# Performance work log

Hardware: AMD Instinct MI355X
Metric: run time of the kernel (lower is better)

Reference implementation:

```python
import jax, jax.numpy as jnp
import numpy as np

B, S, DIM, NH, NKV, HD, HID, L, VOCAB = 1, 2048, 1024, 16, 8, 64, 2816, 2, 32000
EPS = 1e-5
SCALE = float(HD) ** 0.5
NEG = -255.0  # mask fill value used by executorch example inputs


def setup_inputs() -> dict:
    key = jax.random.key(0)
    ks = jax.random.split(key, 16)
    sd = 0.02
    def rnd(k, shape):
        return jax.random.normal(k, shape, dtype=jnp.float32) * sd
    # rope tables: precompute_freqs_cis(head_dim, max_seq_len)[: -1] -> [S, HD//2]
    inv = 1.0 / (10000.0 ** (np.arange(0, HD, 2, dtype=np.float32) / HD))
    ang = np.outer(np.arange(S, dtype=np.float32), inv)
    # causal mask [S, S]
    tril = np.tril(np.ones((S, S), dtype=bool))
    mask = np.where(tril, 0.0, NEG).astype(np.float32)
    return {
        "tokens": jax.random.randint(ks[0], (B, S), 0, VOCAB, dtype=jnp.int32),
        "atten_mask": jnp.asarray(mask),
        "freqs_cos": jnp.asarray(np.cos(ang)),
        "freqs_sin": jnp.asarray(np.sin(ang)),
        "tok_emb": rnd(ks[1], (VOCAB, DIM)),
        "wq": rnd(ks[2], (L, DIM, NH * HD)),
        "wk": rnd(ks[3], (L, DIM, NKV * HD)),
        "wv": rnd(ks[4], (L, DIM, NKV * HD)),
        "wo": rnd(ks[5], (L, NH * HD, DIM)),
        "attn_norm_w": jnp.ones((L, DIM), jnp.float32),
        "ffn_norm_w": jnp.ones((L, DIM), jnp.float32),
        "w1": rnd(ks[6], (L, DIM, HID)),
        "w2": rnd(ks[7], (L, HID, DIM)),
        "w3": rnd(ks[8], (L, DIM, HID)),
        "final_norm_w": jnp.ones((DIM,), jnp.float32),
        "out_w": rnd(ks[9], (DIM, VOCAB)),
    }


def _rmsnorm(x, w):
    return x * jax.lax.rsqrt(jnp.mean(x * x, axis=-1, keepdims=True) + EPS) * w


def _rope(x, c, s):
    # faithful to apply_rotary_emb_single: de-interleave, rotate, concat halves
    xr, xi = x[..., ::2], x[..., 1::2]          # [B,S,H,HD/2]
    c = c[None, :, None, :]
    s = s[None, :, None, :]
    return jnp.concatenate([xr * c - xi * s, xr * s + xi * c], axis=-1)


def reference(tokens, atten_mask, freqs_cos, freqs_sin, tok_emb, wq, wk, wv, wo,
              attn_norm_w, ffn_norm_w, w1, w2, w3, final_norm_w, out_w):
    rep = NH // NKV
    h = tok_emb[tokens]                           # [B,S,DIM]
    k_news, v_news = [], []
    for l in range(L):
        x = _rmsnorm(h, attn_norm_w[l])
        q = (x @ wq[l]).reshape(B, S, NH, HD)
        k = (x @ wk[l]).reshape(B, S, NKV, HD)
        v = (x @ wv[l]).reshape(B, S, NKV, HD)
        q = _rope(q, freqs_cos, freqs_sin)
        k = _rope(k, freqs_cos, freqs_sin)
        # GQA: each kv head serves NH//NKV query heads
        kr = jnp.repeat(k, rep, axis=2)           # [B,S,NH,HD]
        vr = jnp.repeat(v, rep, axis=2)
        attn = jnp.einsum('bshd,bthd->bhst', q, kr) / SCALE + atten_mask[None, None]
        p = jax.nn.softmax(attn, axis=-1)
        y = jnp.einsum('bhst,bthd->bshd', p, vr).reshape(B, S, NH * HD)
        h = h + y @ wo[l]
        x = _rmsnorm(h, ffn_norm_w[l])
        h = h + (jax.nn.silu(x @ w1[l]) * (x @ w3[l])) @ w2[l]
        # output_new_cache_only: last-position rotated K and raw V per kv head
        k_news.append(k[:, -1])                   # [B,NKV,HD]
        v_news.append(v[:, -1])
    logits = _rmsnorm(h, final_norm_w) @ out_w    # [B,S,VOCAB]
    return logits, jnp.stack(k_news), jnp.stack(v_news)
```

## Files before the change

kernel.cpp:

```cpp
#include <hip/hip_runtime.h>
#include <hip/hip_bf16.h>

typedef __bf16 bf16x8 __attribute__((ext_vector_type(8)));
typedef float f32x4 __attribute__((ext_vector_type(4)));
typedef unsigned short ushort4v __attribute__((ext_vector_type(4)));
typedef unsigned short ushort8v __attribute__((ext_vector_type(8)));

#define S_LEN 2048
#define DIM 1024
#define NH 16
#define NKV 8
#define HD 64
#define HID 2816

__device__ __forceinline__ unsigned short f2bf(float f) {
    union { float f; unsigned u; } v; v.f = f;
    unsigned r = v.u + 0x7fffu + ((v.u >> 16) & 1u);
    return (unsigned short)(r >> 16);
}
__device__ __forceinline__ float bf2f(unsigned short u) {
    union { unsigned u; float f; } v; v.u = (unsigned)u << 16; return v.f;
}

__device__ __forceinline__ void gload16(const unsigned short* g, unsigned short* l) {
    __builtin_amdgcn_global_load_lds(
        (const __attribute__((address_space(1))) unsigned int*)g,
        (__attribute__((address_space(3))) unsigned int*)l,
        16, 0, 0);
}

union Frag { f32x4 f; bf16x8 h; };

__device__ __forceinline__ f32x4 lds_read_b128(unsigned addr) {
    f32x4 d;
    asm volatile("ds_read_b128 %0, %1" : "=v"(d) : "v"(addr));
    return d;
}

#define BAR()  asm volatile("s_barrier" ::: "memory")
#define WAITV(n) asm volatile("s_waitcnt vmcnt(" #n ")" ::: "memory")
#define LGKM0() do { asm volatile("s_waitcnt lgkmcnt(0)" ::: "memory"); __builtin_amdgcn_sched_barrier(0); } while (0)

__global__ __launch_bounds__(256) void embed_kernel(const int* __restrict__ tokens,
                                                    const float* __restrict__ emb,
                                                    float* __restrict__ h) {
    int s = blockIdx.x;
    int t = tokens[s];
    float4 v = *(const float4*)&emb[(size_t)t * DIM + threadIdx.x * 4];
    *(float4*)&h[(size_t)s * DIM + threadIdx.x * 4] = v;
}

__global__ __launch_bounds__(256) void rmsnorm_kernel(const float* __restrict__ x,
                                                      const float* __restrict__ w,
                                                      unsigned short* __restrict__ out) {
    __shared__ float sred[4];
    int s = blockIdx.x;
    int tid = threadIdx.x;
    float4 v = *(const float4*)&x[(size_t)s * DIM + tid * 4];
    float ss = v.x * v.x + v.y * v.y + v.z * v.z + v.w * v.w;
#pragma unroll
    for (int off = 32; off; off >>= 1) ss += __shfl_down(ss, off);
    if ((tid & 63) == 0) sred[tid >> 6] = ss;
    __syncthreads();
    float tot = sred[0] + sred[1] + sred[2] + sred[3];
    float scale = rsqrtf(tot * (1.0f / DIM) + 1e-5f);
    float4 wv = *(const float4*)&w[tid * 4];
    ushort4v o;
    o[0] = f2bf(v.x * scale * wv.x); o[1] = f2bf(v.y * scale * wv.y);
    o[2] = f2bf(v.z * scale * wv.z); o[3] = f2bf(v.w * scale * wv.w);
    *(ushort4v*)&out[(size_t)s * DIM + tid * 4] = o;
}

__global__ __launch_bounds__(256) void transpose_w(const float* __restrict__ in,
                                                   unsigned short* __restrict__ out,
                                                   int K, int N) {
    __shared__ unsigned short t[64][68];
    int n0 = blockIdx.x * 64, k0 = blockIdx.y * 64;
    int tid = threadIdx.x;
    int tn = tid & 15, tk = tid >> 4;
#pragma unroll
    for (int p = 0; p < 4; ++p) {
        int k = tk + p * 16;
        float4 v = *(const float4*)&in[(size_t)(k0 + k) * N + n0 + tn * 4];
        t[tn * 4 + 0][k] = f2bf(v.x);
        t[tn * 4 + 1][k] = f2bf(v.y);
        t[tn * 4 + 2][k] = f2bf(v.z);
        t[tn * 4 + 3][k] = f2bf(v.w);
    }
    __syncthreads();
    int wk = tid & 15, wn = tid >> 4;
#pragma unroll
    for (int p = 0; p < 4; ++p) {
        int n = wn + p * 16;
        ushort4v v;
        v[0] = t[n][wk * 4]; v[1] = t[n][wk * 4 + 1];
        v[2] = t[n][wk * 4 + 2]; v[3] = t[n][wk * 4 + 3];
        *(ushort4v*)&out[(size_t)(n0 + n) * K + k0 + wk * 4] = v;
    }
}

__global__ __launch_bounds__(256) void transpose_v(const unsigned short* __restrict__ in,
                                                   unsigned short* __restrict__ out) {
    __shared__ unsigned short t[64][72];
    int c0 = blockIdx.x * 64, s0 = blockIdx.y * 64;
    int tid = threadIdx.x;
    int tc = tid & 15, ts = tid >> 4;
#pragma unroll
    for (int p = 0; p < 4; ++p) {
        int s = ts + p * 16;
        ushort4v v = *(const ushort4v*)&in[(size_t)(s0 + s) * 512 + c0 + tc * 4];
        t[tc * 4 + 0][s] = v[0];
        t[tc * 4 + 1][s] = v[1];
        t[tc * 4 + 2][s] = v[2];
        t[tc * 4 + 3][s] = v[3];
    }
    __syncthreads();
    int ws_ = tid & 15, wc = tid >> 4;
#pragma unroll
    for (int p = 0; p < 4; ++p) {
        int c = wc + p * 16;
        ushort4v v;
        v[0] = t[c][ws_ * 4]; v[1] = t[c][ws_ * 4 + 1];
        v[2] = t[c][ws_ * 4 + 2]; v[3] = t[c][ws_ * 4 + 3];
        *(ushort4v*)&out[(size_t)(c0 + c) * 2048 + s0 + ws_ * 4] = v;
    }
}

__global__ __launch_bounds__(256) void gemm_tn(const unsigned short* __restrict__ A, int lda,
                                               const unsigned short* __restrict__ Bt,
                                               float* __restrict__ Cf,
                                               unsigned short* __restrict__ Cb,
                                               const float* __restrict__ addsrc,
                                               int N, int K) {
    __shared__ unsigned short As[128 * 64];
    __shared__ unsigned short Bs[128 * 64];
    int tid = threadIdx.x;
    int lane = tid & 63;
    int wid = tid >> 6;
    int wrow = wid >> 1, wcol = wid & 1;
    int lr = lane & 15, lg = lane >> 4;
    const int m0 = blockIdx.x * 128, n0 = blockIdx.y * 128;

    const int col8 = (((lane & 7) ^ ((lane >> 3) & 7)) * 8);
    const unsigned short* aG = A + (size_t)(m0 + wid * 32 + (lane >> 3)) * lda + col8;
    const unsigned short* bG = Bt + (size_t)(n0 + wid * 32 + (lane >> 3)) * K + col8;
    unsigned short* aL = As + wid * 2048;
    unsigned short* bL = Bs + wid * 2048;

    f32x4 acc[4][4] = {};

    for (int k0 = 0; k0 < K; k0 += 64) {
#pragma unroll
        for (int i = 0; i < 4; ++i)
            gload16(aG + (size_t)(i * 8) * lda + k0, aL + i * 512);
#pragma unroll
        for (int i = 0; i < 4; ++i)
            gload16(bG + (size_t)(i * 8) * K + k0, bL + i * 512);
        __syncthreads();
#pragma unroll
        for (int kk = 0; kk < 2; ++kk) {
            const int slot = ((kk * 4 + lg) ^ (lr & 7)) * 8;
            bf16x8 aF[4], bF[4];
#pragma unroll
            for (int mi = 0; mi < 4; ++mi)
                aF[mi] = *(const bf16x8*)&As[(wrow * 64 + mi * 16 + lr) * 64 + slot];
#pragma unroll
            for (int ni = 0; ni < 4; ++ni)
                bF[ni] = *(const bf16x8*)&Bs[(wcol * 64 + ni * 16 + lr) * 64 + slot];
#pragma unroll
            for (int mi = 0; mi < 4; ++mi)
#pragma unroll
                for (int ni = 0; ni < 4; ++ni)
                    acc[mi][ni] = __builtin_amdgcn_mfma_f32_16x16x32_bf16(aF[mi], bF[ni], acc[mi][ni], 0, 0, 0);
        }
        __syncthreads();
    }
#pragma unroll
    for (int mi = 0; mi < 4; ++mi)
#pragma unroll
        for (int ni = 0; ni < 4; ++ni) {
            int row = m0 + wrow * 64 + mi * 16 + lg * 4;
            int col = n0 + wcol * 64 + ni * 16 + lr;
#pragma unroll
            for (int r = 0; r < 4; ++r) {
                size_t idx = (size_t)(row + r) * N + col;
                float v = acc[mi][ni][r];
                if (addsrc) v += addsrc[idx];
                if (Cb) Cb[idx] = f2bf(v);
                else    Cf[idx] = v;
            }
        }
}

__global__ __launch_bounds__(256) void gemm_tn64(const unsigned short* __restrict__ A, int lda,
                                                 const unsigned short* __restrict__ Bt,
                                                 float* __restrict__ Cf,
                                                 unsigned short* __restrict__ Cb,
                                                 const float* __restrict__ addsrc,
                                                 int N, int K) {
    __shared__ unsigned short As[64 * 64];
    __shared__ unsigned short Bs[128 * 64];
    int tid = threadIdx.x;
    int lane = tid & 63;
    int wid = tid >> 6;
    int lr = lane & 15, lg = lane >> 4;
    const int m0 = blockIdx.x * 64, n0 = blockIdx.y * 128;

    const int srow = tid >> 3;
    const int col8 = (((tid & 7) ^ ((tid >> 3) & 7)) * 8);
    const unsigned short* aG = A + (size_t)(m0 + srow) * lda + col8;
    const unsigned short* bG = Bt + (size_t)(n0 + srow) * K + col8;
    unsigned short* aL = As + wid * 512;
    unsigned short* bL = Bs + wid * 512;

    f32x4 acc[4][2] = {};

    for (int k0 = 0; k0 < K; k0 += 64) {
        gload16(aG + k0, aL);
        gload16(aG + (size_t)32 * lda + k0, aL + 2048);
#pragma unroll
        for (int i = 0; i < 4; ++i)
            gload16(bG + (size_t)(i * 32) * K + k0, bL + i * 2048);
        __syncthreads();
#pragma unroll
        for (int kk = 0; kk < 2; ++kk) {
            const int slot = ((kk * 4 + lg) ^ (lr & 7)) * 8;
            bf16x8 aF[4], bF[2];
#pragma unroll
            for (int mi = 0; mi < 4; ++mi)
                aF[mi] = *(const bf16x8*)&As[(mi * 16 + lr) * 64 + slot];
#pragma unroll
            for (int ni = 0; ni < 2; ++ni)
                bF[ni] = *(const bf16x8*)&Bs[(wid * 32 + ni * 16 + lr) * 64 + slot];
#pragma unroll
            for (int mi = 0; mi < 4; ++mi)
#pragma unroll
                for (int ni = 0; ni < 2; ++ni)
                    acc[mi][ni] = __builtin_amdgcn_mfma_f32_16x16x32_bf16(aF[mi], bF[ni], acc[mi][ni], 0, 0, 0);
        }
        __syncthreads();
    }
#pragma unroll
    for (int mi = 0; mi < 4; ++mi)
#pragma unroll
        for (int ni = 0; ni < 2; ++ni) {
            int row = m0 + mi * 16 + lg * 4;
            int col = n0 + wid * 32 + ni * 16 + lr;
#pragma unroll
            for (int r = 0; r < 4; ++r) {
                size_t idx = (size_t)(row + r) * N + col;
                float v = acc[mi][ni][r];
                if (addsrc) v += addsrc[idx];
                if (Cb) Cb[idx] = f2bf(v);
                else    Cf[idx] = v;
            }
        }
}

__global__ __launch_bounds__(512) void gemm8(const unsigned short* __restrict__ A,
                                             const unsigned short* __restrict__ Bt,
                                             float* __restrict__ Cf,
                                             unsigned short* __restrict__ Cb,
                                             int N, int K) {
    __shared__ unsigned short ldsbuf[65536];
    const int NT = K >> 6;
    int tid = threadIdx.x;
    int lane = tid & 63;
    int wid = tid >> 6;
    int wm = wid >> 2, wn = wid & 3;
    int lr = lane & 15, lg = lane >> 4;
    int wl = blockIdx.x * gridDim.y + blockIdx.y;
    const int m0 = (wl & 7) * 256, n0 = (wl >> 3) * 256;

    unsigned lds0 = (unsigned)(size_t)(__attribute__((address_space(3))) unsigned short*)ldsbuf;
    const unsigned xoff = (unsigned)((lg ^ ((lr >> 1) & 3)) * 16);
    const int gsw = (lane & 3) ^ ((lane >> 3) & 3);
    const int srow = wid * 16 + (lane >> 2);

#define STAGE(buf, ab, s, t) do {                                                   \
        const unsigned short* _src = (ab) ? Bt : A;                                 \
        int _r0 = (ab) ? n0 : m0;                                                   \
        unsigned short* _l = ldsbuf + (((buf) * 2 + (ab)) * 2 + (s)) * 8192 + wid * 512; \
        const unsigned short* _g = _src + (size_t)(_r0 + srow) * K + (size_t)(t) * 64 + (s) * 32 + gsw * 8; \
        gload16(_g, _l);                                                            \
        gload16(_g + (size_t)128 * K, _l + 4096);                                   \
    } while (0)

    f32x4 acc[8][4] = {};

    STAGE(0, 0, 0, 0); STAGE(0, 1, 0, 0);
    STAGE(0, 0, 1, 0); STAGE(0, 1, 1, 0);
    STAGE(1, 0, 0, 1); STAGE(1, 1, 0, 1);
    WAITV(8);
    BAR();

    for (int t = 0; t < NT; ++t) {
        int buf = t & 1;
        unsigned aBase = lds0 + (unsigned)(buf * 65536) + (unsigned)((wm * 128 + lr) * 64) + xoff;
        unsigned bBase = lds0 + (unsigned)(buf * 65536 + 32768) + (unsigned)((wn * 64 + lr) * 64) + xoff;
        Frag aF[4], bF[4];
#pragma unroll
        for (int s = 0; s < 2; ++s) {
#pragma unroll
            for (int ni = 0; ni < 4; ++ni)
                bF[ni].f = lds_read_b128(bBase + (unsigned)(s * 16384 + ni * 1024));
#pragma unroll
            for (int mi = 0; mi < 4; ++mi)
                aF[mi].f = lds_read_b128(aBase + (unsigned)(s * 16384 + mi * 1024));
            if (s == 0) { if (t + 1 < NT) STAGE(buf ^ 1, 0, 1, t + 1); }
            else        { if (t + 2 < NT) STAGE(buf,     0, 0, t + 2); }
            BAR();
            LGKM0();
            __builtin_amdgcn_s_setprio(1);
#pragma unroll
            for (int mi = 0; mi < 4; ++mi)
#pragma unroll
                for (int ni = 0; ni < 4; ++ni)
                    acc[mi][ni] = __builtin_amdgcn_mfma_f32_16x16x32_bf16(aF[mi].h, bF[ni].h, acc[mi][ni], 0, 0, 0);
            __builtin_amdgcn_s_setprio(0);
            BAR();
#pragma unroll
            for (int mi = 0; mi < 4; ++mi)
                aF[mi].f = lds_read_b128(aBase + (unsigned)(4096 + s * 16384 + mi * 1024));
            if (s == 0) { if (t + 1 < NT) STAGE(buf ^ 1, 1, 1, t + 1); }
            else        { if (t + 2 < NT) STAGE(buf,     1, 0, t + 2); }
            BAR();
            LGKM0();
            __builtin_amdgcn_s_setprio(1);
#pragma unroll
            for (int mi = 0; mi < 4; ++mi)
#pragma unroll
                for (int ni = 0; ni < 4; ++ni)
                    acc[4 + mi][ni] = __builtin_amdgcn_mfma_f32_16x16x32_bf16(aF[mi].h, bF[ni].h, acc[4 + mi][ni], 0, 0, 0);
            __builtin_amdgcn_s_setprio(0);
            if (s == 0) {
                if (t + 1 < NT) { WAITV(8); } else { WAITV(0); }
            } else {
                if (t + 2 < NT)      { WAITV(8); }
                else if (t + 1 < NT) { WAITV(4); }
            }
            BAR();
        }
    }
#undef STAGE

#pragma unroll
    for (int mi = 0; mi < 8; ++mi)
#pragma unroll
        for (int ni = 0; ni < 4; ++ni) {
            int row = m0 + wm * 128 + mi * 16 + lg * 4;
            int col = n0 + wn * 64 + ni * 16 + lr;
#pragma unroll
            for (int r = 0; r < 4; ++r) {
                size_t idx = (size_t)(row + r) * N + col;
                float v = acc[mi][ni][r];
                if (Cb) Cb[idx] = f2bf(v);
                else    Cf[idx] = v;
            }
        }
}

__global__ __launch_bounds__(256) void rope_kernel(const float* __restrict__ qkv,
                                                   const float* __restrict__ fc,
                                                   const float* __restrict__ fs,
                                                   unsigned short* __restrict__ qb,
                                                   unsigned short* __restrict__ kb,
                                                   unsigned short* __restrict__ vb,
                                                   float* __restrict__ out, int layer) {
    const size_t LOGITS = (size_t)S_LEN * 32000;
    int s = blockIdx.x * 4 + (threadIdx.x >> 6);
    int hh = blockIdx.y;
    int lane = threadIdx.x & 63;
    const float* base = qkv + (size_t)s * 2048;
    if (hh < NH) {
        if (lane < 32) {
            const float* row = base + hh * HD;
            float2 x2 = *(const float2*)&row[2 * lane];
            float c = fc[s * 32 + lane], sn = fs[s * 32 + lane];
            size_t o = (size_t)s * (NH * HD) + hh * HD + lane;
            qb[o] = f2bf(x2.x * c - x2.y * sn);
            qb[o + 32] = f2bf(x2.x * sn + x2.y * c);
        }
    } else if (hh < NH + NKV) {
        int kh = hh - NH;
        if (lane < 32) {
            const float* row = base + 1024 + kh * HD;
            float2 x2 = *(const float2*)&row[2 * lane];
            float c = fc[s * 32 + lane], sn = fs[s * 32 + lane];
            float o0 = x2.x * c - x2.y * sn, o1 = x2.x * sn + x2.y * c;
            size_t o = (size_t)s * (NKV * HD) + kh * HD + lane;
            kb[o] = f2bf(o0);
            kb[o + 32] = f2bf(o1);
            if (s == S_LEN - 1) {
                float* kn = out + LOGITS + (size_t)layer * (NKV * HD) + kh * HD;
                kn[lane] = o0; kn[lane + 32] = o1;
            }
        }
    } else {
        int vh = hh - NH - NKV;
        const float* row = base + 1536 + vh * HD;
        float val = row[lane];
        vb[(size_t)s * (NKV * HD) + vh * HD + lane] = f2bf(val);
        if (s == S_LEN - 1)
            out[LOGITS + (size_t)2 * (NKV * HD) + (size_t)layer * (NKV * HD) + vh * HD + lane] = val;
    }
}

__global__ __launch_bounds__(512) void attn_kernel(const unsigned short* __restrict__ qb,
                                                   const unsigned short* __restrict__ kb,
                                                   const unsigned short* __restrict__ vT,
                                                   unsigned short* __restrict__ yb) {
    __shared__ unsigned short Klds[2][4096];
    __shared__ unsigned short Vlds[2][4096];
    __shared__ unsigned short P[8][16 * 72];
    int kvh = blockIdx.x;
    int qt64 = blockIdx.y;
    int tid = threadIdx.x;
    int lane = tid & 63;
    int w = tid >> 6;
    int hq = w & 1, qsub = w >> 1;
    int h = kvh * 2 + hq;
    int lr = lane & 15, lg = lane >> 4;
    int qbase = qt64 * 64 + qsub * 16;
    int qrow = qbase + lr;

    const int sr = tid >> 3;
    const int scol8 = (((tid & 7) ^ ((tid >> 3) & 7)) * 8);
    const int NT = qt64 + 1;

#define STAGEKV(buf, kt) do { \
        gload16(&kb[(size_t)((kt) * 64 + sr) * (NKV * HD) + kvh * 64 + scol8], &Klds[buf][w * 512]); \
        gload16(&vT[(size_t)(kvh * 64 + sr) * 2048 + (kt) * 64 + scol8], &Vlds[buf][w * 512]); \
    } while (0)

    bf16x8 bq[2];
#pragma unroll
    for (int c = 0; c < 2; ++c)
        bq[c] = *(const bf16x8*)&qb[(size_t)qrow * (NH * HD) + h * HD + c * 32 + lg * 8];

    f32x4 O[4] = {};
    float mstate = -1e30f, lstate = 0.f;

    STAGEKV(0, 0);
    WAITV(0);
    BAR();

    for (int kt = 0; kt < NT; ++kt) {
        int buf = kt & 1;
        if (kt + 1 < NT) STAGEKV(buf ^ 1, kt + 1);
        f32x4 s[4];
#pragma unroll
        for (int kc = 0; kc < 4; ++kc) {
            int krl = kc * 16 + lr;
            const unsigned short* kp = &Klds[buf][krl * 64];
            bf16x8 ak0 = *(const bf16x8*)&kp[((lg ^ (lr & 7)) * 8)];
            bf16x8 ak1 = *(const bf16x8*)&kp[(((4 + lg) ^ (lr & 7)) * 8)];
            f32x4 z = {};
            z = __builtin_amdgcn_mfma_f32_16x16x32_bf16(ak0, bq[0], z, 0, 0, 0);
            z = __builtin_amdgcn_mfma_f32_16x16x32_bf16(ak1, bq[1], z, 0, 0, 0);
            s[kc] = z;
        }
        float tm = -1e30f;
#pragma unroll
        for (int kc = 0; kc < 4; ++kc)
#pragma unroll
            for (int r = 0; r < 4; ++r) {
                int key = kt * 64 + kc * 16 + lg * 4 + r;
                float val = s[kc][r] * 0.125f;
                if (key > qrow) val = -1e30f;
                s[kc][r] = val;
                tm = fmaxf(tm, val);
            }
        tm = fmaxf(tm, __shfl_xor(tm, 16));
        tm = fmaxf(tm, __shfl_xor(tm, 32));
        float mn = fmaxf(mstate, tm);
        float sc = __expf(mstate - mn);
        float rs = 0.f;
        ushort4v pk[4];
#pragma unroll
        for (int kc = 0; kc < 4; ++kc)
#pragma unroll
            for (int r = 0; r < 4; ++r) {
                float pf = __expf(s[kc][r] - mn);
                rs += pf;
                pk[kc][r] = f2bf(pf);
            }
        rs += __shfl_xor(rs, 16);
        rs += __shfl_xor(rs, 32);
        lstate = lstate * sc + rs;
        mstate = mn;
        float osc[4];
#pragma unroll
        for (int r = 0; r < 4; ++r)
            osc[r] = __shfl(sc, lg * 4 + r);
#pragma unroll
        for (int n = 0; n < 4; ++n)
#pragma unroll
            for (int r = 0; r < 4; ++r)
                O[n][r] *= osc[r];
#pragma unroll
        for (int kc = 0; kc < 4; ++kc)
            *(ushort4v*)&P[w][lr * 72 + kc * 16 + lg * 4] = pk[kc];
        bf16x8 pa[2];
#pragma unroll
        for (int g = 0; g < 2; ++g)
            pa[g] = *(const bf16x8*)&P[w][lr * 72 + g * 32 + lg * 8];
#pragma unroll
        for (int n = 0; n < 4; ++n) {
            const unsigned short* vp = &Vlds[buf][(n * 16 + lr) * 64];
#pragma unroll
            for (int g = 0; g < 2; ++g) {
                bf16x8 bv = *(const bf16x8*)&vp[(((g * 4 + lg) ^ (lr & 7)) * 8)];
                O[n] = __builtin_amdgcn_mfma_f32_16x16x32_bf16(pa[g], bv, O[n], 0, 0, 0);
            }
        }
        if (kt + 1 < NT) WAITV(0);
        LGKM0();
        BAR();
    }
#undef STAGEKV

    float linv[4];
#pragma unroll
    for (int r = 0; r < 4; ++r)
        linv[r] = 1.f / __shfl(lstate, lg * 4 + r);
#pragma unroll
    for (int n = 0; n < 4; ++n)
#pragma unroll
        for (int r = 0; r < 4; ++r) {
            int row = qbase + lg * 4 + r;
            yb[(size_t)row * (NH * HD) + h * HD + n * 16 + lr] = f2bf(O[n][r] * linv[r]);
        }
}

__global__ __launch_bounds__(256) void silu_mul_kernel(unsigned short* __restrict__ gu) {
    size_t idx = (size_t)blockIdx.x * 256 + threadIdx.x;
    int s = (int)(idx / 352);
    int c8 = (int)(idx % 352);
    unsigned short* gp = gu + (size_t)s * 5632 + c8 * 8;
    ushort8v a = *(const ushort8v*)gp;
    ushort8v b = *(const ushort8v*)(gp + 2816);
#pragma unroll
    for (int j = 0; j < 8; ++j) {
        float x = bf2f(a[j]), y = bf2f(b[j]);
        a[j] = f2bf(x / (1.f + __expf(-x)) * y);
    }
    *(ushort8v*)gp = a;
}

extern "C" void kernel_launch(void* const* d_in, const int* in_sizes, int n_in,
                              void* d_out, int out_size, void* d_ws, size_t ws_size,
                              hipStream_t stream) {
    const int* tokens = (const int*)d_in[0];
    const float* freqs_cos = (const float*)d_in[2];
    const float* freqs_sin = (const float*)d_in[3];
    const float* tok_emb = (const float*)d_in[4];
    const float* wq = (const float*)d_in[5];
    const float* wk = (const float*)d_in[6];
    const float* wv = (const float*)d_in[7];
    const float* wo = (const float*)d_in[8];
    const float* attn_norm_w = (const float*)d_in[9];
    const float* ffn_norm_w = (const float*)d_in[10];
    const float* w1 = (const float*)d_in[11];
    const float* w2 = (const float*)d_in[12];
    const float* w3 = (const float*)d_in[13];
    const float* final_norm_w = (const float*)d_in[14];
    const float* out_w = (const float*)d_in[15];
    float* out = (float*)d_out;

    const size_t SD = (size_t)S_LEN * DIM;
    const size_t SKV = (size_t)S_LEN * NKV * HD;

    char* p = (char*)d_ws;
    auto take = [&](size_t bytes) { char* r = p; p += (bytes + 255) & ~(size_t)255; return r; };
    float* h            = (float*)take(SD * 4);
    unsigned short* xnb = (unsigned short*)take(SD * 2);
    char* uni = p;
    float* qkvf         = (float*)uni;
    unsigned short* qb  = (unsigned short*)(uni + 17039360);
    unsigned short* kb  = qb + SD;
    unsigned short* vb  = kb + SKV;
    unsigned short* vT  = vb + SKV;
    unsigned short* ybv = vT + SKV;
    unsigned short* gu  = ybv + SD;
    unsigned short* wT  = gu + (size_t)S_LEN * 5632;
    unsigned short* owT = (unsigned short*)uni;

    embed_kernel<<<S_LEN, 256, 0, stream>>>(tokens, tok_emb, h);
    for (int l = 0; l < 2; ++l) {
        rmsnorm_kernel<<<S_LEN, 256, 0, stream>>>(h, attn_norm_w + l * DIM, xnb);
        transpose_w<<<dim3(16, 16), 256, 0, stream>>>(wq + (size_t)l * DIM * 1024, wT, DIM, 1024);
        transpose_w<<<dim3(8, 16), 256, 0, stream>>>(wk + (size_t)l * DIM * 512, wT + (size_t)1024 * DIM, DIM, 512);
        transpose_w<<<dim3(8, 16), 256, 0, stream>>>(wv + (size_t)l * DIM * 512, wT + (size_t)1536 * DIM, DIM, 512);
        gemm_tn<<<dim3(16, 16), 256, 0, stream>>>(xnb, DIM, wT, qkvf, nullptr, nullptr, 2048, DIM);
        rope_kernel<<<dim3(S_LEN / 4, 32), 256, 0, stream>>>(qkvf, freqs_cos, freqs_sin, qb, kb, vb, out, l);
        transpose_v<<<dim3(8, 32), 256, 0, stream>>>(vb, vT);
        attn_kernel<<<dim3(NKV, S_LEN / 64), 512, 0, stream>>>(qb, kb, vT, ybv);
        transpose_w<<<dim3(16, 16), 256, 0, stream>>>(wo + (size_t)l * 1024 * DIM, wT, 1024, DIM);
        gemm_tn64<<<dim3(32, 8), 256, 0, stream>>>(ybv, 1024, wT, h, nullptr, h, DIM, 1024);
        rmsnorm_kernel<<<S_LEN, 256, 0, stream>>>(h, ffn_norm_w + l * DIM, xnb);
        transpose_w<<<dim3(44, 16), 256, 0, stream>>>(w1 + (size_t)l * DIM * HID, wT, DIM, HID);
        transpose_w<<<dim3(44, 16), 256, 0, stream>>>(w3 + (size_t)l * DIM * HID, wT + (size_t)HID * DIM, DIM, HID);
        gemm8<<<dim3(8, 22), 512, 0, stream>>>(xnb, wT, nullptr, gu, 5632, DIM);
        silu_mul_kernel<<<(S_LEN * 352) / 256, 256, 0, stream>>>(gu);
        transpose_w<<<dim3(16, 44), 256, 0, stream>>>(w2 + (size_t)l * HID * 1024, wT, HID, 1024);
        gemm_tn64<<<dim3(32, 8), 256, 0, stream>>>(gu, 5632, wT, h, nullptr, h, DIM, HID);
    }
    rmsnorm_kernel<<<S_LEN, 256, 0, stream>>>(h, final_norm_w, xnb);
    transpose_w<<<dim3(500, 16), 256, 0, stream>>>(out_w, owT, DIM, 32000);
    gemm8<<<dim3(8, 125), 512, 0, stream>>>(xnb, owT, out, nullptr, 32000, DIM);
}
```

Baseline: 688.5 us.

## Fuse SiLU into FFN GEMM epilogue, merge transposes, retile attention

Several changes at once. The w1/w3 weights are interleaved row-wise so the gate/up GEMM epilogue can pair outputs with a lane shuffle and write silu(g)*u directly, which removes the separate silu kernel and halves the gu buffer. The q/k/v and w1/w3 weight transposes are merged into single launches, and the V conversion plus transpose now reads straight from the fp32 QKV output, which drops the vb round trip. Attention moves to 256-thread blocks over 32-row query strips, scheduled heaviest-first to balance causal work. The risk is lower per-block parallelism in attention and some wasted early-exit blocks in the merged qkv transpose.

```diff
diff --git a/kernel.cpp b/kernel.cpp
--- a/kernel.cpp
+++ b/kernel.cpp
@@ -12,6 +12,7 @@
 #define NKV 8
 #define HD 64
 #define HID 2816
+#define LOGITS ((size_t)S_LEN * 32000)
 
 __device__ __forceinline__ unsigned short f2bf(float f) {
     union { float f; unsigned u; } v; v.f = f;
@@ -71,11 +72,11 @@
     *(ushort4v*)&out[(size_t)s * DIM + tid * 4] = o;
 }
 
-__global__ __launch_bounds__(256) void transpose_w(const float* __restrict__ in,
-                                                   unsigned short* __restrict__ out,
-                                                   int K, int N) {
+__device__ __forceinline__ void tpose_body(const float* __restrict__ in,
+                                           unsigned short* __restrict__ out,
+                                           int K, int N, int n0, int k0,
+                                           int rowMul, int rowOff) {
     __shared__ unsigned short t[64][68];
-    int n0 = blockIdx.x * 64, k0 = blockIdx.y * 64;
     int tid = threadIdx.x;
     int tn = tid & 15, tk = tid >> 4;
 #pragma unroll
@@ -95,12 +96,38 @@
         ushort4v v;
         v[0] = t[n][wk * 4]; v[1] = t[n][wk * 4 + 1];
         v[2] = t[n][wk * 4 + 2]; v[3] = t[n][wk * 4 + 3];
-        *(ushort4v*)&out[(size_t)(n0 + n) * K + k0 + wk * 4] = v;
-    }
-}
-
-__global__ __launch_bounds__(256) void transpose_v(const unsigned short* __restrict__ in,
-                                                   unsigned short* __restrict__ out) {
+        *(ushort4v*)&out[(size_t)(rowMul * (n0 + n) + rowOff) * K + k0 + wk * 4] = v;
+    }
+}
+
+__global__ __launch_bounds__(256) void transpose_w(const float* __restrict__ in,
+                                                   unsigned short* __restrict__ out,
+                                                   int K, int N) {
+    tpose_body(in, out, K, N, blockIdx.x * 64, blockIdx.y * 64, 1, 0);
+}
+
+__global__ __launch_bounds__(256) void transpose_qkv(const float* __restrict__ wq,
+                                                     const float* __restrict__ wk,
+                                                     const float* __restrict__ wv,
+                                                     unsigned short* __restrict__ out) {
+    int z = blockIdx.z;
+    if (z > 0 && blockIdx.x >= 8) return;
+    const float* in = z == 0 ? wq : (z == 1 ? wk : wv);
+    int N = z == 0 ? 1024 : 512;
+    int rowOff = z == 0 ? 0 : (z == 1 ? 1024 : 1536);
+    tpose_body(in, out, DIM, N, blockIdx.x * 64, blockIdx.y * 64, 1, rowOff);
+}
+
+__global__ __launch_bounds__(256) void transpose_w13(const float* __restrict__ w1,
+                                                     const float* __restrict__ w3,
+                                                     unsigned short* __restrict__ out) {
+    int z = blockIdx.z;
+    tpose_body(z ? w3 : w1, out, DIM, HID, blockIdx.x * 64, blockIdx.y * 64, 2, z);
+}
+
+__global__ __launch_bounds__(256) void transpose_vf(const float* __restrict__ qkvf,
+                                                    unsigned short* __restrict__ vT,
+                                                    float* __restrict__ out, int layer) {
     __shared__ unsigned short t[64][72];
     int c0 = blockIdx.x * 64, s0 = blockIdx.y * 64;
     int tid = threadIdx.x;
@@ -108,11 +135,15 @@
 #pragma unroll
     for (int p = 0; p < 4; ++p) {
         int s = ts + p * 16;
-        ushort4v v = *(const ushort4v*)&in[(size_t)(s0 + s) * 512 + c0 + tc * 4];
-        t[tc * 4 + 0][s] = v[0];
-        t[tc * 4 + 1][s] = v[1];
-        t[tc * 4 + 2][s] = v[2];
-        t[tc * 4 + 3][s] = v[3];
+        float4 v = *(const float4*)&qkvf[(size_t)(s0 + s) * 2048 + 1536 + c0 + tc * 4];
+        t[tc * 4 + 0][s] = f2bf(v.x);
+        t[tc * 4 + 1][s] = f2bf(v.y);
+        t[tc * 4 + 2][s] = f2bf(v.z);
+        t[tc * 4 + 3][s] = f2bf(v.w);
+        if (s0 + s == S_LEN - 1) {
+            float* vn = out + LOGITS + 2 * (NKV * HD) + (size_t)layer * (NKV * HD) + c0 + tc * 4;
+            vn[0] = v.x; vn[1] = v.y; vn[2] = v.z; vn[3] = v.w;
+        }
     }
     __syncthreads();
     int ws_ = tid & 15, wc = tid >> 4;
@@ -122,7 +153,7 @@
         ushort4v v;
         v[0] = t[c][ws_ * 4]; v[1] = t[c][ws_ * 4 + 1];
         v[2] = t[c][ws_ * 4 + 2]; v[3] = t[c][ws_ * 4 + 3];
-        *(ushort4v*)&out[(size_t)(c0 + c) * 2048 + s0 + ws_ * 4] = v;
+        *(ushort4v*)&vT[(size_t)(c0 + c) * 2048 + s0 + ws_ * 4] = v;
     }
 }
 
@@ -257,6 +288,7 @@
         }
 }
 
+template<int FUSE>
 __global__ __launch_bounds__(512) void gemm8(const unsigned short* __restrict__ A,
                                              const unsigned short* __restrict__ Bt,
                                              float* __restrict__ Cf,
@@ -352,10 +384,16 @@
             int col = n0 + wn * 64 + ni * 16 + lr;
 #pragma unroll
             for (int r = 0; r < 4; ++r) {
-                size_t idx = (size_t)(row + r) * N + col;
                 float v = acc[mi][ni][r];
-                if (Cb) Cb[idx] = f2bf(v);
-                else    Cf[idx] = v;
+                if (FUSE) {
+                    float o = __shfl_xor(v, 1);
+                    if (!(lr & 1)) {
+                        float res = v / (1.f + __expf(-v)) * o;
+                        Cb[(size_t)(row + r) * (HID) + (col >> 1)] = f2bf(res);
+                    }
+                } else {
+                    Cf[(size_t)(row + r) * N + col] = v;
+                }
             }
         }
 }
@@ -365,72 +403,62 @@
                                                    const float* __restrict__ fs,
                                                    unsigned short* __restrict__ qb,
                                                    unsigned short* __restrict__ kb,
-                                                   unsigned short* __restrict__ vb,
                                                    float* __restrict__ out, int layer) {
-    const size_t LOGITS = (size_t)S_LEN * 32000;
     int s = blockIdx.x * 4 + (threadIdx.x >> 6);
     int hh = blockIdx.y;
     int lane = threadIdx.x & 63;
+    if (lane >= 32) return;
     const float* base = qkv + (size_t)s * 2048;
     if (hh < NH) {
-        if (lane < 32) {
-            const float* row = base + hh * HD;
-            float2 x2 = *(const float2*)&row[2 * lane];
-            float c = fc[s * 32 + lane], sn = fs[s * 32 + lane];
-            size_t o = (size_t)s * (NH * HD) + hh * HD + lane;
-            qb[o] = f2bf(x2.x * c - x2.y * sn);
-            qb[o + 32] = f2bf(x2.x * sn + x2.y * c);
-        }
-    } else if (hh < NH + NKV) {
+        const float* row = base + hh * HD;
+        float2 x2 = *(const float2*)&row[2 * lane];
+        float c = fc[s * 32 + lane], sn = fs[s * 32 + lane];
+        size_t o = (size_t)s * (NH * HD) + hh * HD + lane;
+        qb[o] = f2bf(x2.x * c - x2.y * sn);
+        qb[o + 32] = f2bf(x2.x * sn + x2.y * c);
+    } else {
         int kh = hh - NH;
-        if (lane < 32) {
-            const float* row = base + 1024 + kh * HD;
-            float2 x2 = *(const float2*)&row[2 * lane];
-            float c = fc[s * 32 + lane], sn = fs[s * 32 + lane];
-            float o0 = x2.x * c - x2.y * sn, o1 = x2.x * sn + x2.y * c;
-            size_t o = (size_t)s * (NKV * HD) + kh * HD + lane;
-            kb[o] = f2bf(o0);
-            kb[o + 32] = f2bf(o1);
-            if (s == S_LEN - 1) {
-                float* kn = out + LOGITS + (size_t)layer * (NKV * HD) + kh * HD;
-                kn[lane] = o0; kn[lane + 32] = o1;
-            }
-        }
-    } else {
-        int vh = hh - NH - NKV;
-        const float* row = base + 1536 + vh * HD;
-        float val = row[lane];
-        vb[(size_t)s * (NKV * HD) + vh * HD + lane] = f2bf(val);
-        if (s == S_LEN - 1)
-            out[LOGITS + (size_t)2 * (NKV * HD) + (size_t)layer * (NKV * HD) + vh * HD + lane] = val;
-    }
-}
-
-__global__ __launch_bounds__(512) void attn_kernel(const unsigned short* __restrict__ qb,
+        const float* row = base + 1024 + kh * HD;
+        float2 x2 = *(const float2*)&row[2 * lane];
+        float c = fc[s * 32 + lane], sn = fs[s * 32 + lane];
+        float o0 = x2.x * c - x2.y * sn, o1 = x2.x * sn + x2.y * c;
+        size_t o = (size_t)s * (NKV * HD) + kh * HD + lane;
+        kb[o] = f2bf(o0);
+        kb[o + 32] = f2bf(o1);
+        if (s == S_LEN - 1) {
+            float* kn = out + LOGITS + (size_t)layer * (NKV * HD) + kh * HD;
+            kn[lane] = o0; kn[lane + 32] = o1;
+        }
+    }
+}
+
+__global__ __launch_bounds__(256) void attn_kernel(const unsigned short* __restrict__ qb,
                                                    const unsigned short* __restrict__ kb,
                                                    const unsigned short* __restrict__ vT,
                                                    unsigned short* __restrict__ yb) {
     __shared__ unsigned short Klds[2][4096];
     __shared__ unsigned short Vlds[2][4096];
-    __shared__ unsigned short P[8][16 * 72];
+    __shared__ unsigned short P[4][16 * 72];
     int kvh = blockIdx.x;
-    int qt64 = blockIdx.y;
+    int strip = 63 - blockIdx.y;
     int tid = threadIdx.x;
     int lane = tid & 63;
     int w = tid >> 6;
     int hq = w & 1, qsub = w >> 1;
     int h = kvh * 2 + hq;
     int lr = lane & 15, lg = lane >> 4;
-    int qbase = qt64 * 64 + qsub * 16;
+    int qbase = strip * 32 + qsub * 16;
     int qrow = qbase + lr;
 
     const int sr = tid >> 3;
-    const int scol8 = (((tid & 7) ^ ((tid >> 3) & 7)) * 8);
-    const int NT = qt64 + 1;
+    const int scol8 = (((tid & 7) ^ (sr & 7)) * 8);
+    const int NT = (strip >> 1) + 1;
 
 #define STAGEKV(buf, kt) do { \
-        gload16(&kb[(size_t)((kt) * 64 + sr) * (NKV * HD) + kvh * 64 + scol8], &Klds[buf][w * 512]); \
+        gload16(&kb[(size_t)((kt) * 64 + sr) * 512 + kvh * 64 + scol8], &Klds[buf][w * 512]); \
+        gload16(&kb[(size_t)((kt) * 64 + sr + 32) * 512 + kvh * 64 + scol8], &Klds[buf][2048 + w * 512]); \
         gload16(&vT[(size_t)(kvh * 64 + sr) * 2048 + (kt) * 64 + scol8], &Vlds[buf][w * 512]); \
+        gload16(&vT[(size_t)(kvh * 64 + sr + 32) * 2048 + (kt) * 64 + scol8], &Vlds[buf][2048 + w * 512]); \
     } while (0)
 
     bf16x8 bq[2];
@@ -531,21 +559,6 @@
             int row = qbase + lg * 4 + r;
             yb[(size_t)row * (NH * HD) + h * HD + n * 16 + lr] = f2bf(O[n][r] * linv[r]);
         }
-}
-
-__global__ __launch_bounds__(256) void silu_mul_kernel(unsigned short* __restrict__ gu) {
-    size_t idx = (size_t)blockIdx.x * 256 + threadIdx.x;
-    int s = (int)(idx / 352);
-    int c8 = (int)(idx % 352);
-    unsigned short* gp = gu + (size_t)s * 5632 + c8 * 8;
-    ushort8v a = *(const ushort8v*)gp;
-    ushort8v b = *(const ushort8v*)(gp + 2816);
-#pragma unroll
-    for (int j = 0; j < 8; ++j) {
-        float x = bf2f(a[j]), y = bf2f(b[j]);
-        a[j] = f2bf(x / (1.f + __expf(-x)) * y);
-    }
-    *(ushort8v*)gp = a;
 }
 
 extern "C" void kernel_launch(void* const* d_in, const int* in_sizes, int n_in,
@@ -579,34 +592,31 @@
     float* qkvf         = (float*)uni;
     unsigned short* qb  = (unsigned short*)(uni + 17039360);
     unsigned short* kb  = qb + SD;
-    unsigned short* vb  = kb + SKV;
-    unsigned short* vT  = vb + SKV;
+    unsigned short* vT  = kb + SKV;
     unsigned short* ybv = vT + SKV;
     unsigned short* gu  = ybv + SD;
-    unsigned short* wT  = gu + (size_t)S_LEN * 5632;
+    unsigned short* wT  = gu + (size_t)S_LEN * HID;
     unsigned short* owT = (unsigned short*)uni;
 
     embed_kernel<<<S_LEN, 256, 0, stream>>>(tokens, tok_emb, h);
     for (int l = 0; l < 2; ++l) {
         rmsnorm_kernel<<<S_LEN, 256, 0, stream>>>(h, attn_norm_w + l * DIM, xnb);
-        transpose_w<<<dim3(16, 16), 256, 0, stream>>>(wq + (size_t)l * DIM * 1024, wT, DIM, 1024);
-        transpose_w<<<dim3(8, 16), 256, 0, stream>>>(wk + (size_t)l * DIM * 512, wT + (size_t)1024 * DIM, DIM, 512);
-        transpose_w<<<dim3(8, 16), 256, 0, stream>>>(wv + (size_t)l * DIM * 512, wT + (size_t)1536 * DIM, DIM, 512);
+        transpose_qkv<<<dim3(16, 16, 3), 256, 0, stream>>>(
+            wq + (size_t)l * DIM * 1024, wk + (size_t)l * DIM * 512, wv + (size_t)l * DIM * 512, wT);
         gemm_tn<<<dim3(16, 16), 256, 0, stream>>>(xnb, DIM, wT, qkvf, nullptr, nullptr, 2048, DIM);
-        rope_kernel<<<dim3(S_LEN / 4, 32), 256, 0, stream>>>(qkvf, freqs_cos, freqs_sin, qb, kb, vb, out, l);
-        transpose_v<<<dim3(8, 32), 256, 0, stream>>>(vb, vT);
-        attn_kernel<<<dim3(NKV, S_LEN / 64), 512, 0, stream>>>(qb, kb, vT, ybv);
+        rope_kernel<<<dim3(S_LEN / 4, 24), 256, 0, stream>>>(qkvf, freqs_cos, freqs_sin, qb, kb, out, l);
+        transpose_vf<<<dim3(8, 32), 256, 0, stream>>>(qkvf, vT, out, l);
+        attn_kernel<<<dim3(NKV, 64), 256, 0, stream>>>(qb, kb, vT, ybv);
         transpose_w<<<dim3(16, 16), 256, 0, stream>>>(wo + (size_t)l * 1024 * DIM, wT, 1024, DIM);
         gemm_tn64<<<dim3(32, 8), 256, 0, stream>>>(ybv, 1024, wT, h, nullptr, h, DIM, 1024);
         rmsnorm_kernel<<<S_LEN, 256, 0, stream>>>(h, ffn_norm_w + l * DIM, xnb);
-        transpose_w<<<dim3(44, 16), 256, 0, stream>>>(w1 + (size_t)l * DIM * HID, wT, DIM, HID);
-        transpose_w<<<dim3(44, 16), 256, 0, stream>>>(w3 + (size_t)l * DIM * HID, wT + (size_t)HID * DIM, DIM, HID);
-        gemm8<<<dim3(8, 22), 512, 0, stream>>>(xnb, wT, nullptr, gu, 5632, DIM);
-        silu_mul_kernel<<<(S_LEN * 352) / 256, 256, 0, stream>>>(gu);
+        transpose_w13<<<dim3(44, 16, 2), 256, 0, stream>>>(
+            w1 + (size_t)l * DIM * HID, w3 + (size_t)l * DIM * HID, wT);
+        gemm8<1><<<dim3(8, 22), 512, 0, stream>>>(xnb, wT, nullptr, gu, 5632, DIM);
         transpose_w<<<dim3(16, 44), 256, 0, stream>>>(w2 + (size_t)l * HID * 1024, wT, HID, 1024);
-        gemm_tn64<<<dim3(32, 8), 256, 0, stream>>>(gu, 5632, wT, h, nullptr, h, DIM, HID);
+        gemm_tn64<<<dim3(32, 8), 256, 0, stream>>>(gu, HID, wT, h, nullptr, h, DIM, HID);
     }
     rmsnorm_kernel<<<S_LEN, 256, 0, stream>>>(h, final_norm_w, xnb);
     transpose_w<<<dim3(500, 16), 256, 0, stream>>>(out_w, owT, DIM, 32000);
-    gemm8<<<dim3(8, 125), 512, 0, stream>>>(xnb, owT, out, nullptr, 32000, DIM);
-}
+    gemm8<0><<<dim3(8, 125), 512, 0, stream>>>(xnb, owT, out, nullptr, 32000, DIM);
+}
```

Result: faster. 669.5 us (-2.8%).
